# Optimization experiments

Measured on AMD Instinct MI355X. Metric: run time of the kernel, lower is better.

## Reference

```python
import jax, jax.numpy as jnp
import numpy as np

N_NODES = 100000
N_EDGES = 600000
D = 128


def gcn_conv(x, W, b, src, dst, n_nodes):
    """PyG-style GCNConv: add self-loops, symmetric deg^{-1/2} normalization."""
    xw = x @ W  # [N, out]
    # degree of destination nodes, counting the added self-loop
    deg = jnp.zeros((n_nodes,), xw.dtype).at[dst].add(1.0) + 1.0
    dinv = jax.lax.rsqrt(deg)
    coef = dinv[src] * dinv[dst]  # [E]
    agg = jnp.zeros_like(xw).at[dst].add(xw[src] * coef[:, None])
    agg = agg + xw * (dinv * dinv)[:, None]  # self-loop term
    return agg + b


def setup_inputs() -> dict:
    key = jax.random.key(0)
    k = jax.random.split(key, 9)
    s = 1.0 / np.sqrt(D)
    return {
        "x": jax.random.normal(k[0], (N_NODES, D), jnp.float32),
        "edge_index_pos": jax.random.randint(k[1], (2, N_EDGES), 0, N_NODES, jnp.int64),
        "edge_index_neg": jax.random.randint(k[2], (2, N_EDGES), 0, N_NODES, jnp.int64),
        "W1": jax.random.uniform(k[3], (D, D), jnp.float32, -s, s),
        "b1": jnp.zeros((D,), jnp.float32),
        "W2": jax.random.uniform(k[4], (D, D), jnp.float32, -s, s),
        "b2": jnp.zeros((D,), jnp.float32),
        "weight": jax.random.uniform(k[5], (2 * D, D), jnp.float32, -s, s),
        "bias": jnp.zeros((D,), jnp.float32),
    }


def reference(x, edge_index_pos, edge_index_neg, W1, b1, W2, b2, weight, bias):
    n = x.shape[0]
    h1 = gcn_conv(x, W1, b1, edge_index_pos[0], edge_index_pos[1], n)  # [N, D]
    h2 = gcn_conv(x, W2, b2, edge_index_neg[0], edge_index_neg[1], n)  # [N, D]
    h = jnp.concatenate([h1, h2], axis=-1)  # [N, 2D]
    return h @ weight + bias  # [N, D]
```

## Files before the change

kernel.cpp:

```cpp
#include <hip/hip_runtime.h>

#define N_NODES 100000
#define NT (2 * N_NODES)
#define D 128
#define N_EDGES 600000
#define ET (2 * N_EDGES)
#define SCAN_B 256
#define NBLK2 ((NT + SCAN_B - 1) / SCAN_B)
#define FBLK ((N_NODES + 127) / 128)

typedef __attribute__((ext_vector_type(8))) short bf16x8;
typedef __attribute__((ext_vector_type(4))) float f32x4;

__device__ __forceinline__ unsigned short f2bf(float f) {
    union { float f; unsigned u; } v; v.f = f;
    unsigned r = (v.u + 0x7fff + ((v.u >> 16) & 1)) >> 16;
    return (unsigned short)r;
}
__device__ __forceinline__ float bf2f(unsigned short h) {
    union { unsigned u; float f; } v; v.u = ((unsigned)h) << 16;
    return v.f;
}

__device__ __forceinline__ long long load_idx(const void* e, long long i, int is32) {
    if (is32) return (long long)((const int*)e)[i];
    return ((const long long*)e)[i];
}

__global__ void detect_kernel(const unsigned long long* __restrict__ e, int* __restrict__ flag) {
    if (threadIdx.x == 0 && blockIdx.x == 0) {
        int is32 = 0;
        for (int i = 0; i < 64; ++i) {
            if (e[i] > 0xFFFFFFFFull) { is32 = 1; break; }
        }
        *flag = is32;
    }
}

__global__ void x2bf_kernel(const float* __restrict__ x, unsigned short* __restrict__ xb) {
    long long t = (long long)blockIdx.x * blockDim.x + threadIdx.x;
    if (t >= (long long)N_NODES * 32) return;
    float4 a = ((const float4*)x)[t];
    ((ushort4*)xb)[t] = make_ushort4(f2bf(a.x), f2bf(a.y), f2bf(a.z), f2bf(a.w));
}

__global__ void prep_Mt(const float* __restrict__ W1, const float* __restrict__ W2,
                        const float* __restrict__ weight, unsigned short* __restrict__ Mt) {
    int idx = blockIdx.x * blockDim.x + threadIdx.x;
    int j = idx >> 8, k = idx & 255;
    float a = 0.f;
    if (k < D) {
        for (int d = 0; d < D; ++d) a += W1[k * D + d] * weight[d * D + j];
    } else {
        for (int d = 0; d < D; ++d) a += W2[(k - D) * D + d] * weight[(D + d) * D + j];
    }
    Mt[j * 256 + k] = f2bf(a);
}

__global__ void prep_bt(const float* __restrict__ b1, const float* __restrict__ b2,
                        const float* __restrict__ weight, const float* __restrict__ bias,
                        float* __restrict__ bt) {
    int j = threadIdx.x;
    if (j >= D) return;
    float a = bias[j];
    for (int k = 0; k < D; ++k)
        a += b1[k] * weight[k * D + j] + b2[k] * weight[(D + k) * D + j];
    bt[j] = a;
}

__global__ void degree_both(const void* __restrict__ ep, const void* __restrict__ en,
                            const int* __restrict__ flag, int* __restrict__ degi) {
    int i = blockIdx.x * blockDim.x + threadIdx.x;
    if (i >= ET) return;
    int is32 = *flag;
    int conv = (i >= N_EDGES);
    const void* e = conv ? en : ep;
    int j = conv ? i - N_EDGES : i;
    long long d = load_idx(e, (long long)N_EDGES + j, is32);
    atomicAdd(&degi[conv * N_NODES + (int)d], 1);
}

__global__ void scan_pass1(const int* __restrict__ degi, int* __restrict__ bsum,
                           float* __restrict__ dinv) {
    __shared__ int sm[SCAN_B];
    int i = blockIdx.x * SCAN_B + threadIdx.x;
    int v = (i < NT) ? degi[i] : 0;
    if (i < NT) dinv[i] = rsqrtf((float)v + 1.0f);
    sm[threadIdx.x] = v;
    __syncthreads();
    for (int s = SCAN_B / 2; s > 0; s >>= 1) {
        if (threadIdx.x < s) sm[threadIdx.x] += sm[threadIdx.x + s];
        __syncthreads();
    }
    if (threadIdx.x == 0) bsum[blockIdx.x] = sm[0];
}

__global__ void scan_pass2(int* __restrict__ bsum) {
    __shared__ int sm[1024];
    int t = threadIdx.x;
    int v = (t < NBLK2) ? bsum[t] : 0;
    sm[t] = v;
    __syncthreads();
    for (int ofs = 1; ofs < 1024; ofs <<= 1) {
        int add = (t >= ofs) ? sm[t - ofs] : 0;
        __syncthreads();
        sm[t] += add;
        __syncthreads();
    }
    if (t < NBLK2) bsum[t] = sm[t] - v;
}

__global__ void scan_pass3(const int* __restrict__ degi, const int* __restrict__ bsum,
                           int* __restrict__ off) {
    __shared__ int sm[SCAN_B];
    int i = blockIdx.x * SCAN_B + threadIdx.x;
    int v = (i < NT) ? degi[i] : 0;
    sm[threadIdx.x] = v;
    __syncthreads();
    for (int ofs = 1; ofs < SCAN_B; ofs <<= 1) {
        int add = (threadIdx.x >= ofs) ? sm[threadIdx.x - ofs] : 0;
        __syncthreads();
        sm[threadIdx.x] += add;
        __syncthreads();
    }
    int excl = sm[threadIdx.x] - v + bsum[blockIdx.x];
    if (i < NT) off[i] = excl;
    if (i == NT - 1) off[NT] = excl + v;
}

__global__ void csr_fill_both(const void* __restrict__ ep, const void* __restrict__ en,
                              const int* __restrict__ flag, const int* __restrict__ off,
                              int* __restrict__ degi, const float* __restrict__ dinv,
                              int2* __restrict__ csr) {
    int i = blockIdx.x * blockDim.x + threadIdx.x;
    if (i >= ET) return;
    int is32 = *flag;
    int conv = (i >= N_EDGES);
    const void* e = conv ? en : ep;
    int j = conv ? i - N_EDGES : i;
    int si = (int)load_idx(e, j, is32);
    int di = (int)load_idx(e, (long long)N_EDGES + j, is32);
    int g = conv * N_NODES;
    int node = g + di;
    int pos = off[node] + atomicSub(&degi[node], 1) - 1;
    float coef = dinv[g + si] * dinv[node];
    csr[pos] = make_int2(si, __float_as_int(coef));
}

__global__ __launch_bounds__(512) void fused_gather_gemm(
    const int* __restrict__ off, const int2* __restrict__ csr,
    const unsigned short* __restrict__ xb, const float* __restrict__ dinv,
    const unsigned short* __restrict__ Mt, const float* __restrict__ bt,
    float* __restrict__ out) {
    __shared__ unsigned short mlds[128][264];
    int t = threadIdx.x;
    for (int c = t; c < 4096; c += 512) {
        int row = c >> 5;
        int kc = (c & 31) * 8;
        *(ulonglong2*)&mlds[row][kc] = *(const ulonglong2*)&Mt[row * 256 + kc];
    }
    __syncthreads();

    int wave = t >> 6, lane = t & 63;
    int rl = lane & 15, q = lane >> 4;
    int gr = blockIdx.x * 128 + wave * 16 + rl;
    const bool valid = gr < N_NODES;

    bf16x8 af[8];
    #pragma unroll
    for (int conv = 0; conv < 2; ++conv) {
        float acc[4][8];
        if (valid) {
            int n = conv * N_NODES + gr;
            float dn = dinv[n];
            float f = dn * dn;
            const unsigned short* xr = xb + (size_t)gr * D + q * 8;
            #pragma unroll
            for (int m = 0; m < 4; ++m) {
                bf16x8 v = *(const bf16x8*)(xr + m * 32);
                #pragma unroll
                for (int j = 0; j < 8; ++j) acc[m][j] = bf2f((unsigned short)v[j]) * f;
            }
            int e0 = off[n], e1 = off[n + 1];
            for (int e = e0; e < e1; ++e) {
                int2 sc = csr[e];
                float coef = __int_as_float(sc.y);
                const unsigned short* xs = xb + (size_t)sc.x * D + q * 8;
                #pragma unroll
                for (int m = 0; m < 4; ++m) {
                    bf16x8 v = *(const bf16x8*)(xs + m * 32);
                    #pragma unroll
                    for (int j = 0; j < 8; ++j) acc[m][j] += coef * bf2f((unsigned short)v[j]);
                }
            }
        } else {
            #pragma unroll
            for (int m = 0; m < 4; ++m)
                #pragma unroll
                for (int j = 0; j < 8; ++j) acc[m][j] = 0.f;
        }
        #pragma unroll
        for (int m = 0; m < 4; ++m) {
            bf16x8 a;
            #pragma unroll
            for (int j = 0; j < 8; ++j) a[j] = (short)f2bf(acc[m][j]);
            af[conv * 4 + m] = a;
        }
    }

    f32x4 C[8];
    #pragma unroll
    for (int i = 0; i < 8; ++i) C[i] = (f32x4){0.f, 0.f, 0.f, 0.f};
    #pragma unroll
    for (int ks = 0; ks < 8; ++ks) {
        bf16x8 afr = af[ks];
        #pragma unroll
        for (int ct = 0; ct < 8; ++ct) {
            bf16x8 bfr = *(const bf16x8*)&mlds[ct * 16 + rl][ks * 32 + q * 8];
            C[ct] = __builtin_amdgcn_mfma_f32_16x16x32_bf16(afr, bfr, C[ct], 0, 0, 0);
        }
    }

    int orow = blockIdx.x * 128 + wave * 16 + q * 4;
    #pragma unroll
    for (int ct = 0; ct < 8; ++ct) {
        int col = ct * 16 + rl;
        float b = bt[col];
        #pragma unroll
        for (int reg = 0; reg < 4; ++reg) {
            int row = orow + reg;
            if (row < N_NODES) out[(long long)row * D + col] = C[ct][reg] + b;
        }
    }
}

extern "C" void kernel_launch(void* const* d_in, const int* in_sizes, int n_in,
                              void* d_out, int out_size, void* d_ws, size_t ws_size,
                              hipStream_t stream) {
    const float* x      = (const float*)d_in[0];
    const void*  e_pos  = d_in[1];
    const void*  e_neg  = d_in[2];
    const float* W1     = (const float*)d_in[3];
    const float* b1     = (const float*)d_in[4];
    const float* W2     = (const float*)d_in[5];
    const float* b2     = (const float*)d_in[6];
    const float* weight = (const float*)d_in[7];
    const float* bias   = (const float*)d_in[8];
    float* out = (float*)d_out;

    unsigned short* xb = (unsigned short*)d_ws;
    unsigned short* Mt = xb + (size_t)N_NODES * D;
    float* bt   = (float*)(Mt + 128 * 256);
    float* dinv = bt + D;
    int*   flag = (int*)(dinv + NT);
    int*   degi = flag + 4;
    int*   off  = degi + NT;
    int*   bsum = off + NT + 4;
    int2*  csr  = (int2*)(bsum + 1024);

    detect_kernel<<<1, 64, 0, stream>>>((const unsigned long long*)e_pos, flag);
    x2bf_kernel<<<12500, 256, 0, stream>>>(x, xb);
    prep_Mt<<<(128 * 256) / 256, 256, 0, stream>>>(W1, W2, weight, Mt);
    prep_bt<<<1, D, 0, stream>>>(b1, b2, weight, bias, bt);

    hipMemsetAsync(degi, 0, NT * sizeof(int), stream);
    const int egrid = (ET + 255) / 256;
    degree_both<<<egrid, 256, 0, stream>>>(e_pos, e_neg, flag, degi);
    scan_pass1<<<NBLK2, SCAN_B, 0, stream>>>(degi, bsum, dinv);
    scan_pass2<<<1, 1024, 0, stream>>>(bsum);
    scan_pass3<<<NBLK2, SCAN_B, 0, stream>>>(degi, bsum, off);
    csr_fill_both<<<egrid, 256, 0, stream>>>(e_pos, e_neg, flag, off, degi, dinv, csr);

    fused_gather_gemm<<<FBLK, 512, 0, stream>>>(off, csr, xb, dinv, Mt, bt, out);
}
```

Measured before the change: 240.6 us.

## Merge prep kernels, parallelize detect, enlarge gather blocks, prefetch CSR entries

```diff
diff --git a/kernel.cpp b/kernel.cpp
--- a/kernel.cpp
+++ b/kernel.cpp
@@ -7,7 +7,8 @@
 #define ET (2 * N_EDGES)
 #define SCAN_B 256
 #define NBLK2 ((NT + SCAN_B - 1) / SCAN_B)
-#define FBLK ((N_NODES + 127) / 128)
+#define FROWS 256
+#define FBLK ((N_NODES + FROWS - 1) / FROWS)
 
 typedef __attribute__((ext_vector_type(8))) short bf16x8;
 typedef __attribute__((ext_vector_type(4))) float f32x4;
@@ -28,56 +29,53 @@
 }
 
 __global__ void detect_kernel(const unsigned long long* __restrict__ e, int* __restrict__ flag) {
-    if (threadIdx.x == 0 && blockIdx.x == 0) {
-        int is32 = 0;
-        for (int i = 0; i < 64; ++i) {
-            if (e[i] > 0xFFFFFFFFull) { is32 = 1; break; }
-        }
-        *flag = is32;
-    }
-}
-
-__global__ void x2bf_kernel(const float* __restrict__ x, unsigned short* __restrict__ xb) {
-    long long t = (long long)blockIdx.x * blockDim.x + threadIdx.x;
-    if (t >= (long long)N_NODES * 32) return;
-    float4 a = ((const float4*)x)[t];
-    ((ushort4*)xb)[t] = make_ushort4(f2bf(a.x), f2bf(a.y), f2bf(a.z), f2bf(a.w));
-}
-
-__global__ void prep_Mt(const float* __restrict__ W1, const float* __restrict__ W2,
-                        const float* __restrict__ weight, unsigned short* __restrict__ Mt) {
-    int idx = blockIdx.x * blockDim.x + threadIdx.x;
-    int j = idx >> 8, k = idx & 255;
-    float a = 0.f;
-    if (k < D) {
-        for (int d = 0; d < D; ++d) a += W1[k * D + d] * weight[d * D + j];
+    unsigned long long v = e[threadIdx.x];
+    unsigned long long m = __ballot(v > 0xFFFFFFFFull);
+    if (threadIdx.x == 0) *flag = (m != 0ull) ? 1 : 0;
+}
+
+__global__ void prep_weights(const float* __restrict__ W1, const float* __restrict__ W2,
+                             const float* __restrict__ weight,
+                             const float* __restrict__ b1, const float* __restrict__ b2,
+                             const float* __restrict__ bias,
+                             unsigned short* __restrict__ Mt, float* __restrict__ bt) {
+    if (blockIdx.x < 128) {
+        int idx = blockIdx.x * 256 + threadIdx.x;
+        int j = idx >> 8, k = idx & 255;
+        float a = 0.f;
+        if (k < D) {
+            for (int d = 0; d < D; ++d) a += W1[k * D + d] * weight[d * D + j];
+        } else {
+            for (int d = 0; d < D; ++d) a += W2[(k - D) * D + d] * weight[(D + d) * D + j];
+        }
+        Mt[j * 256 + k] = f2bf(a);
     } else {
-        for (int d = 0; d < D; ++d) a += W2[(k - D) * D + d] * weight[(D + d) * D + j];
-    }
-    Mt[j * 256 + k] = f2bf(a);
-}
-
-__global__ void prep_bt(const float* __restrict__ b1, const float* __restrict__ b2,
-                        const float* __restrict__ weight, const float* __restrict__ bias,
-                        float* __restrict__ bt) {
-    int j = threadIdx.x;
-    if (j >= D) return;
-    float a = bias[j];
-    for (int k = 0; k < D; ++k)
-        a += b1[k] * weight[k * D + j] + b2[k] * weight[(D + k) * D + j];
-    bt[j] = a;
-}
-
-__global__ void degree_both(const void* __restrict__ ep, const void* __restrict__ en,
+        int j = threadIdx.x;
+        if (j >= D) return;
+        float a = bias[j];
+        for (int k = 0; k < D; ++k)
+            a += b1[k] * weight[k * D + j] + b2[k] * weight[(D + k) * D + j];
+        bt[j] = a;
+    }
+}
+
+__global__ void x2bf_degree(const float* __restrict__ x, unsigned short* __restrict__ xb,
+                            const void* __restrict__ ep, const void* __restrict__ en,
                             const int* __restrict__ flag, int* __restrict__ degi) {
-    int i = blockIdx.x * blockDim.x + threadIdx.x;
-    if (i >= ET) return;
-    int is32 = *flag;
-    int conv = (i >= N_EDGES);
-    const void* e = conv ? en : ep;
-    int j = conv ? i - N_EDGES : i;
-    long long d = load_idx(e, (long long)N_EDGES + j, is32);
-    atomicAdd(&degi[conv * N_NODES + (int)d], 1);
+    if (blockIdx.x < 12500) {
+        long long t = (long long)blockIdx.x * 256 + threadIdx.x;
+        float4 a = ((const float4*)x)[t];
+        ((ushort4*)xb)[t] = make_ushort4(f2bf(a.x), f2bf(a.y), f2bf(a.z), f2bf(a.w));
+    } else {
+        int i = (blockIdx.x - 12500) * 256 + threadIdx.x;
+        if (i >= ET) return;
+        int is32 = *flag;
+        int conv = (i >= N_EDGES);
+        const void* e = conv ? en : ep;
+        int j = conv ? i - N_EDGES : i;
+        long long d = load_idx(e, (long long)N_EDGES + j, is32);
+        atomicAdd(&degi[conv * N_NODES + (int)d], 1);
+    }
 }
 
 __global__ void scan_pass1(const int* __restrict__ degi, int* __restrict__ bsum,
@@ -147,14 +145,14 @@
     csr[pos] = make_int2(si, __float_as_int(coef));
 }
 
-__global__ __launch_bounds__(512) void fused_gather_gemm(
+__global__ __launch_bounds__(1024, 8) void fused_gather_gemm(
     const int* __restrict__ off, const int2* __restrict__ csr,
     const unsigned short* __restrict__ xb, const float* __restrict__ dinv,
     const unsigned short* __restrict__ Mt, const float* __restrict__ bt,
     float* __restrict__ out) {
     __shared__ unsigned short mlds[128][264];
     int t = threadIdx.x;
-    for (int c = t; c < 4096; c += 512) {
+    for (int c = t; c < 4096; c += 1024) {
         int row = c >> 5;
         int kc = (c & 31) * 8;
         *(ulonglong2*)&mlds[row][kc] = *(const ulonglong2*)&Mt[row * 256 + kc];
@@ -163,7 +161,7 @@
 
     int wave = t >> 6, lane = t & 63;
     int rl = lane & 15, q = lane >> 4;
-    int gr = blockIdx.x * 128 + wave * 16 + rl;
+    int gr = blockIdx.x * FROWS + wave * 16 + rl;
     const bool valid = gr < N_NODES;
 
     bf16x8 af[8];
@@ -182,15 +180,19 @@
                 for (int j = 0; j < 8; ++j) acc[m][j] = bf2f((unsigned short)v[j]) * f;
             }
             int e0 = off[n], e1 = off[n + 1];
-            for (int e = e0; e < e1; ++e) {
-                int2 sc = csr[e];
-                float coef = __int_as_float(sc.y);
-                const unsigned short* xs = xb + (size_t)sc.x * D + q * 8;
-                #pragma unroll
-                for (int m = 0; m < 4; ++m) {
-                    bf16x8 v = *(const bf16x8*)(xs + m * 32);
+            if (e0 < e1) {
+                int2 sc = csr[e0];
+                for (int e = e0; e < e1; ++e) {
+                    int2 nsc = (e + 1 < e1) ? csr[e + 1] : sc;
+                    float coef = __int_as_float(sc.y);
+                    const unsigned short* xs = xb + (size_t)sc.x * D + q * 8;
                     #pragma unroll
-                    for (int j = 0; j < 8; ++j) acc[m][j] += coef * bf2f((unsigned short)v[j]);
+                    for (int m = 0; m < 4; ++m) {
+                        bf16x8 v = *(const bf16x8*)(xs + m * 32);
+                        #pragma unroll
+                        for (int j = 0; j < 8; ++j) acc[m][j] += coef * bf2f((unsigned short)v[j]);
+                    }
+                    sc = nsc;
                 }
             }
         } else {
@@ -221,7 +223,7 @@
         }
     }
 
-    int orow = blockIdx.x * 128 + wave * 16 + q * 4;
+    int orow = blockIdx.x * FROWS + wave * 16 + q * 4;
     #pragma unroll
     for (int ct = 0; ct < 8; ++ct) {
         int col = ct * 16 + rl;
@@ -259,17 +261,15 @@
     int2*  csr  = (int2*)(bsum + 1024);
 
     detect_kernel<<<1, 64, 0, stream>>>((const unsigned long long*)e_pos, flag);
-    x2bf_kernel<<<12500, 256, 0, stream>>>(x, xb);
-    prep_Mt<<<(128 * 256) / 256, 256, 0, stream>>>(W1, W2, weight, Mt);
-    prep_bt<<<1, D, 0, stream>>>(b1, b2, weight, bias, bt);
-
     hipMemsetAsync(degi, 0, NT * sizeof(int), stream);
+    prep_weights<<<129, 256, 0, stream>>>(W1, W2, weight, b1, b2, bias, Mt, bt);
+
     const int egrid = (ET + 255) / 256;
-    degree_both<<<egrid, 256, 0, stream>>>(e_pos, e_neg, flag, degi);
+    x2bf_degree<<<12500 + egrid, 256, 0, stream>>>(x, xb, e_pos, e_neg, flag, degi);
     scan_pass1<<<NBLK2, SCAN_B, 0, stream>>>(degi, bsum, dinv);
     scan_pass2<<<1, 1024, 0, stream>>>(bsum);
     scan_pass3<<<NBLK2, SCAN_B, 0, stream>>>(degi, bsum, off);
     csr_fill_both<<<egrid, 256, 0, stream>>>(e_pos, e_neg, flag, off, degi, dinv, csr);
 
-    fused_gather_gemm<<<FBLK, 512, 0, stream>>>(off, csr, xb, dinv, Mt, bt, out);
-}
+    fused_gather_gemm<<<FBLK, 1024, 0, stream>>>(off, csr, xb, dinv, Mt, bt, out);
+}
```

Result: slower. 266.3 us (+10.7%).
